# Optimization experiments

Measured on AMD Instinct MI355X. Metric: run time of the kernel, lower is better.

Reference implementation:

```python
import jax, jax.numpy as jnp
import numpy as np

IMAGE_W = 256
IMAGE_H = 256
SIGMA = 0.2
EPS = 1e-07


def _gauss_filter(g, size, psize, pad):
    """g: [B,N] center coords in pixels. Returns [B,N,size,psize]."""
    # grid coords over padded canvas: value i - pad at row i (matches np.indices - pad)
    coords = jnp.arange(size + 2 * pad, dtype=jnp.float32) - pad          # [size+2pad]
    offs = jnp.arange(1, psize + 1, dtype=jnp.float32) - psize / 2 - 0.5  # [psize]
    mu = g[:, :, None] + offs[None, None, :]                              # [B,N,psize]
    F = jnp.exp(-(coords[None, None, :, None] - mu[:, :, None, :]) ** 2 / (2 * SIGMA ** 2))
    F = F / (F.sum(axis=2, keepdims=True) + EPS)
    return F[:, :, pad:size + pad]                                        # [B,N,size,psize]


def setup_inputs() -> dict:
    key = jax.random.key(0)
    k1, k2 = jax.random.split(key)
    brushes = jax.random.uniform(k1, (32, 64, 2), dtype=jnp.float32)
    patches = jax.random.normal(k2, (32, 64, 3, 16, 16), dtype=jnp.float32)
    return {"brushes": brushes, "patches": patches}


def reference(brushes, patches):
    B, N, C, ph, pw = patches.shape
    pad = ph // 2  # pad='half_patch'
    gx = brushes[:, :, 0] * IMAGE_W  # [B,N]
    gy = brushes[:, :, 1] * IMAGE_H
    Fx = _gauss_filter(gx, IMAGE_W, pw, pad)  # [B,N,w,pw]
    Fy = _gauss_filter(gy, IMAGE_H, ph, pad)  # [B,N,h,ph]
    # contract over pw: [B,N,C,w,ph]
    t = jnp.einsum('bnwq,bncpq->bncwp', Fx, patches)
    # contract over ph: [B,N,C,w,h]
    out = jnp.einsum('bncwp,bnhp->bncwh', t, Fy)
    out = out.mean(axis=1)            # [B,C,w,h]
    out = jnp.swapaxes(out, 2, 3)     # [B,C,h,w]
    return out
```

## Files before the change

### kernel.cpp

```cpp
#include <hip/hip_runtime.h>
#include <hip/hip_bf16.h>


#define TILE 16

__global__ __launch_bounds__(256) void brush_tile(
        const float* __restrict__ brushes,
        const float* __restrict__ patches,
        float* __restrict__ out)
{
    const int b   = blockIdx.z;
    const int tx  = blockIdx.x * TILE;
    const int ty  = blockIdx.y * TILE;
    const int tid = threadIdx.x;
    const int qi  = tid & 15;
    const int pi  = tid >> 4;
    const int w   = tx + qi;
    const int h   = ty + pi;

    __shared__ float  gxy[128];
    __shared__ unsigned long long smask;
    __shared__ float  invZ[32];
    __shared__ float4 T4[16 * 21];

    if (tid < 80)
        T4[(tid / 5) * 21 + 16 + (tid % 5)] = make_float4(0, 0, 0, 0);

    if (tid < 64) {
        float2 g = ((const float2*)brushes)[(b << 6) + tid];
        g.x *= 256.0f; g.y *= 256.0f;
        ((float2*)gxy)[tid] = g;
        const bool hit =
            (g.x >= (float)tx - 9.5f) & (g.x <= (float)tx + 24.5f) &
            (g.y >= (float)ty - 9.5f) & (g.y <= (float)ty + 24.5f);
        const unsigned long long m = __ballot(hit);
        if (tid == 0) smask = m;
    }
    __syncthreads();
    unsigned long long mask = smask;

    float acc0 = 0.0f, acc1 = 0.0f, acc2 = 0.0f;
    const float E25 = 1.3887944e-11f;

    while (mask) {
        const int n = __builtin_ctzll(mask);
        mask &= mask - 1;
        const float gx = gxy[2 * n], gy = gxy[2 * n + 1];

        const float* pb = patches + (size_t)((b << 6) + n) * 768;
        const float r0 = pb[tid];
        const float r1 = pb[tid + 256];
        const float r2 = pb[tid + 512];

        if (tid < 32) {
            const int axis = tid >> 4, q = tid & 15;
            const float g  = axis ? gy : gx;
            const float mu = g + (float)q - 7.5f;
            const float fl = floorf(mu);
            float Z = 0.0f;
#pragma unroll
            for (int d = -1; d <= 2; ++d) {
                const float c = fl + (float)d;
                if (c >= -8.0f && c <= 263.0f) {
                    const float u = c - mu;
                    Z += __expf(-12.5f * u * u);
                }
            }
            invZ[tid] = 1.0f / (Z + 1e-7f);
        }
        __syncthreads();

        const float zx = invZ[qi];
        const float v0 = r0 * zx, v1 = r1 * zx, v2 = r2 * zx;

        {
            const float ax  = (float)w - gx + 7.5f;
            const bool  okx = (ax >= -2.5f) & (ax <= 17.5f);
            int qlo = (int)ceilf(ax - 2.0f);
            qlo = qlo < 0 ? 0 : (qlo > 15 ? 15 : qlo);
            float d0 = ax - (float)qlo;
            d0 = fminf(fmaxf(d0, -3.0f), 3.0f);
            float wgt = okx ? __expf(-12.5f * d0 * d0) : 0.0f;
            float u   = __expf(25.0f * d0 - 12.5f);
            const int base = ((pi & 3) << 4) + qlo;
            float4 s = make_float4(0, 0, 0, 0);
#pragma unroll
            for (int j = 0; j < 5; ++j) {
                const float a0 = __shfl(v0, base + j, 64);
                const float a1 = __shfl(v1, base + j, 64);
                const float a2 = __shfl(v2, base + j, 64);
                const float wj = (qlo + j < 16) ? wgt : 0.0f;
                s.x += wj * a0; s.y += wj * a1; s.z += wj * a2;
                wgt *= u; u *= E25;
            }
            const float zy = invZ[16 + pi];
            s.x *= zy; s.y *= zy; s.z *= zy;
            T4[qi * 21 + pi] = s;
        }
        __syncthreads();

        {
            const float ay = (float)h - gy + 7.5f;
            if (ay >= -2.5f && ay <= 17.5f) {
                int plo = (int)ceilf(ay - 2.0f);
                plo = plo < 0 ? 0 : (plo > 15 ? 15 : plo);
                const float d0 = ay - (float)plo;
                float wgt = __expf(-12.5f * d0 * d0);
                float u   = __expf(25.0f * d0 - 12.5f);
                const float4* row = &T4[qi * 21 + plo];
#pragma unroll
                for (int j = 0; j < 5; ++j) {
                    const float4 v = row[j];
                    acc0 += wgt * v.x; acc1 += wgt * v.y; acc2 += wgt * v.z;
                    wgt *= u; u *= E25;
                }
            }
        }
    }

    const float sc = 1.0f / 64.0f;
    float* ob = out + (((size_t)(b * 3)) << 16) + (h << 8) + w;
    ob[0]       = acc0 * sc;
    ob[1 << 16] = acc1 * sc;
    ob[2 << 16] = acc2 * sc;
}

extern "C" void kernel_launch(void* const* d_in, const int* in_sizes, int n_in,
                              void* d_out, int out_size, void* d_ws, size_t ws_size,
                              hipStream_t stream) {
    const float* brushes = (const float*)d_in[0];
    const float* patches = (const float*)d_in[1];
    float* out = (float*)d_out;
    brush_tile<<<dim3(16, 16, 32), dim3(256), 0, stream>>>(brushes, patches, out);
}
```

Measured before the change: 78.54 us.

## Switch from output-tile gather to per-brush scatter with atomic accumulation

Replaces the per-output-tile kernel, which loops over the brushes overlapping each tile, with one block per brush. Each block computes a 22x22 footprint through two separable small contractions in shared memory and accumulates into the output with atomicAdd. A separate zero-fill kernel clears the output first. This removes the serial brush loop and repeated per-tile syncs, at the cost of a second launch, a full output write pass and atomic contention where brushes overlap.

```diff
diff --git a/kernel.cpp b/kernel.cpp
--- a/kernel.cpp
+++ b/kernel.cpp
@@ -1,128 +1,113 @@
 #include <hip/hip_runtime.h>
-#include <hip/hip_bf16.h>
 
 
-#define TILE 16
+__global__ __launch_bounds__(256) void zero_out(float4* __restrict__ out)
+{
+    out[blockIdx.x * 256 + threadIdx.x] = make_float4(0.f, 0.f, 0.f, 0.f);
+}
 
-__global__ __launch_bounds__(256) void brush_tile(
+__global__ __launch_bounds__(256) void brush_scatter(
         const float* __restrict__ brushes,
         const float* __restrict__ patches,
         float* __restrict__ out)
 {
-    const int b   = blockIdx.z;
-    const int tx  = blockIdx.x * TILE;
-    const int ty  = blockIdx.y * TILE;
+    const int n   = blockIdx.x;
+    const int b   = blockIdx.y;
     const int tid = threadIdx.x;
-    const int qi  = tid & 15;
-    const int pi  = tid >> 4;
-    const int w   = tx + qi;
-    const int h   = ty + pi;
 
-    __shared__ float  gxy[128];
-    __shared__ unsigned long long smask;
-    __shared__ float  invZ[32];
-    __shared__ float4 T4[16 * 21];
+    __shared__ float P[3 * 256];
+    __shared__ float wT[2][22][5];
+    __shared__ int   qloT[2][22];
+    __shared__ float T[3 * 352];
 
-    if (tid < 80)
-        T4[(tid / 5) * 21 + 16 + (tid % 5)] = make_float4(0, 0, 0, 0);
+    const int bn = (b << 6) + n;
+    const float gx = brushes[2 * bn]     * 256.0f;
+    const float gy = brushes[2 * bn + 1] * 256.0f;
+    const int x0 = (int)floorf(gx) - 10;
+    const int y0 = (int)floorf(gy) - 10;
 
-    if (tid < 64) {
-        float2 g = ((const float2*)brushes)[(b << 6) + tid];
-        g.x *= 256.0f; g.y *= 256.0f;
-        ((float2*)gxy)[tid] = g;
-        const bool hit =
-            (g.x >= (float)tx - 9.5f) & (g.x <= (float)tx + 24.5f) &
-            (g.y >= (float)ty - 9.5f) & (g.y <= (float)ty + 24.5f);
-        const unsigned long long m = __ballot(hit);
-        if (tid == 0) smask = m;
+    const float* pb = patches + (size_t)bn * 768;
+    P[tid]       = pb[tid];
+    P[tid + 256] = pb[tid + 256];
+    P[tid + 512] = pb[tid + 512];
+
+    if (tid < 220) {
+        const int axis = tid / 110;
+        const int r    = tid - axis * 110;
+        const int i    = r / 5;
+        const int j    = r - i * 5;
+        const float g    = axis ? gy : gx;
+        const float wpos = (float)((axis ? y0 : x0) + i);
+        const float a    = wpos - g + 7.5f;
+        int qlo = (int)ceilf(a - 2.5f);
+        qlo = qlo < 0 ? 0 : (qlo > 11 ? 11 : qlo);
+        const int q = qlo + j;
+        const float mu = g + (float)q - 7.5f;
+        const float fl = floorf(mu);
+        float Z = 0.0f;
+#pragma unroll
+        for (int d = -1; d <= 2; ++d) {
+            const float c = fl + (float)d;
+            if (c >= -8.0f && c <= 263.0f) {
+                const float u = c - mu;
+                Z += __expf(-12.5f * u * u);
+            }
+        }
+        const float dd  = wpos - mu;
+        float wgt = __expf(-12.5f * dd * dd) / (Z + 1e-7f);
+        if (axis == 0) wgt *= 0.015625f;
+        wT[axis][i][j] = wgt;
+        if (j == 0) qloT[axis][i] = qlo;
     }
     __syncthreads();
-    unsigned long long mask = smask;
 
-    float acc0 = 0.0f, acc1 = 0.0f, acc2 = 0.0f;
-    const float E25 = 1.3887944e-11f;
+    for (int it = tid; it < 352; it += 256) {
+        const int p = it / 22;
+        const int i = it - p * 22;
+        const int qlo = qloT[0][i];
+        const float w0 = wT[0][i][0], w1 = wT[0][i][1], w2 = wT[0][i][2],
+                    w3 = wT[0][i][3], w4 = wT[0][i][4];
+        const float* Pp = &P[p * 16 + qlo];
+#pragma unroll
+        for (int c = 0; c < 3; ++c) {
+            const float* Pc = Pp + c * 256;
+            T[c * 352 + p * 22 + i] =
+                w0 * Pc[0] + w1 * Pc[1] + w2 * Pc[2] + w3 * Pc[3] + w4 * Pc[4];
+        }
+    }
+    __syncthreads();
 
-    while (mask) {
-        const int n = __builtin_ctzll(mask);
-        mask &= mask - 1;
-        const float gx = gxy[2 * n], gy = gxy[2 * n + 1];
-
-        const float* pb = patches + (size_t)((b << 6) + n) * 768;
-        const float r0 = pb[tid];
-        const float r1 = pb[tid + 256];
-        const float r2 = pb[tid + 512];
-
-        if (tid < 32) {
-            const int axis = tid >> 4, q = tid & 15;
-            const float g  = axis ? gy : gx;
-            const float mu = g + (float)q - 7.5f;
-            const float fl = floorf(mu);
-            float Z = 0.0f;
-#pragma unroll
-            for (int d = -1; d <= 2; ++d) {
-                const float c = fl + (float)d;
-                if (c >= -8.0f && c <= 263.0f) {
-                    const float u = c - mu;
-                    Z += __expf(-12.5f * u * u);
-                }
+    float* ob = out + ((size_t)(b * 3) << 16);
+    for (int e = tid; e < 484; e += 256) {
+        const int yi = e / 22;
+        const int xi = e - yi * 22;
+        const int h = y0 + yi;
+        const int w = x0 + xi;
+        if (((unsigned)h < 256u) & ((unsigned)w < 256u)) {
+            const int plo = qloT[1][yi];
+            const float w0 = wT[1][yi][0], w1 = wT[1][yi][1], w2 = wT[1][yi][2],
+                        w3 = wT[1][yi][3], w4 = wT[1][yi][4];
+            float v0, v1, v2;
+            {
+                const float* Tc = &T[0 * 352 + plo * 22 + xi];
+                v0 = w0*Tc[0] + w1*Tc[22] + w2*Tc[44] + w3*Tc[66] + w4*Tc[88];
             }
-            invZ[tid] = 1.0f / (Z + 1e-7f);
-        }
-        __syncthreads();
-
-        const float zx = invZ[qi];
-        const float v0 = r0 * zx, v1 = r1 * zx, v2 = r2 * zx;
-
-        {
-            const float ax  = (float)w - gx + 7.5f;
-            const bool  okx = (ax >= -2.5f) & (ax <= 17.5f);
-            int qlo = (int)ceilf(ax - 2.0f);
-            qlo = qlo < 0 ? 0 : (qlo > 15 ? 15 : qlo);
-            float d0 = ax - (float)qlo;
-            d0 = fminf(fmaxf(d0, -3.0f), 3.0f);
-            float wgt = okx ? __expf(-12.5f * d0 * d0) : 0.0f;
-            float u   = __expf(25.0f * d0 - 12.5f);
-            const int base = ((pi & 3) << 4) + qlo;
-            float4 s = make_float4(0, 0, 0, 0);
-#pragma unroll
-            for (int j = 0; j < 5; ++j) {
-                const float a0 = __shfl(v0, base + j, 64);
-                const float a1 = __shfl(v1, base + j, 64);
-                const float a2 = __shfl(v2, base + j, 64);
-                const float wj = (qlo + j < 16) ? wgt : 0.0f;
-                s.x += wj * a0; s.y += wj * a1; s.z += wj * a2;
-                wgt *= u; u *= E25;
+            {
+                const float* Tc = &T[1 * 352 + plo * 22 + xi];
+                v1 = w0*Tc[0] + w1*Tc[22] + w2*Tc[44] + w3*Tc[66] + w4*Tc[88];
             }
-            const float zy = invZ[16 + pi];
-            s.x *= zy; s.y *= zy; s.z *= zy;
-            T4[qi * 21 + pi] = s;
-        }
-        __syncthreads();
-
-        {
-            const float ay = (float)h - gy + 7.5f;
-            if (ay >= -2.5f && ay <= 17.5f) {
-                int plo = (int)ceilf(ay - 2.0f);
-                plo = plo < 0 ? 0 : (plo > 15 ? 15 : plo);
-                const float d0 = ay - (float)plo;
-                float wgt = __expf(-12.5f * d0 * d0);
-                float u   = __expf(25.0f * d0 - 12.5f);
-                const float4* row = &T4[qi * 21 + plo];
-#pragma unroll
-                for (int j = 0; j < 5; ++j) {
-                    const float4 v = row[j];
-                    acc0 += wgt * v.x; acc1 += wgt * v.y; acc2 += wgt * v.z;
-                    wgt *= u; u *= E25;
-                }
+            {
+                const float* Tc = &T[2 * 352 + plo * 22 + xi];
+                v2 = w0*Tc[0] + w1*Tc[22] + w2*Tc[44] + w3*Tc[66] + w4*Tc[88];
+            }
+            if (fabsf(v0) + fabsf(v1) + fabsf(v2) > 1e-12f) {
+                const int off = (h << 8) + w;
+                atomicAdd(ob + off,               v0);
+                atomicAdd(ob + off + (1 << 16),   v1);
+                atomicAdd(ob + off + (2 << 16),   v2);
             }
         }
     }
-
-    const float sc = 1.0f / 64.0f;
-    float* ob = out + (((size_t)(b * 3)) << 16) + (h << 8) + w;
-    ob[0]       = acc0 * sc;
-    ob[1 << 16] = acc1 * sc;
-    ob[2 << 16] = acc2 * sc;
 }
 
 extern "C" void kernel_launch(void* const* d_in, const int* in_sizes, int n_in,
@@ -131,5 +116,6 @@
     const float* brushes = (const float*)d_in[0];
     const float* patches = (const float*)d_in[1];
     float* out = (float*)d_out;
-    brush_tile<<<dim3(16, 16, 32), dim3(256), 0, stream>>>(brushes, patches, out);
+    zero_out<<<dim3(6144), dim3(256), 0, stream>>>((float4*)out);
+    brush_scatter<<<dim3(64, 32), dim3(256), 0, stream>>>(brushes, patches, out);
 }
```

Measured after the change: 81.51 us. 3.8% more time.

## Precompute normalizers for all hit brushes and double-buffer T4 to drop a barrier

Applied to the files above, without the earlier changes.

All normalization factors for the brushes that hit the tile are now computed in parallel before the main loop, using a compacted brush list, instead of by 32 threads inside each iteration. The T4 scratch tile is double-buffered, so each iteration needs one barrier instead of two. Shared memory grows to 8 KB of invZ plus a second T4 buffer, which may reduce occupancy.

```diff
diff --git a/kernel.cpp b/kernel.cpp
--- a/kernel.cpp
+++ b/kernel.cpp
@@ -1,5 +1,4 @@
 #include <hip/hip_runtime.h>
-#include <hip/hip_bf16.h>
 
 
 #define TILE 16
@@ -20,11 +19,14 @@
 
     __shared__ float  gxy[128];
     __shared__ unsigned long long smask;
-    __shared__ float  invZ[32];
-    __shared__ float4 T4[16 * 21];
+    __shared__ unsigned char slist[64];
+    __shared__ float  invZ[64][32];
+    __shared__ float4 T4[2][16 * 21];
 
-    if (tid < 80)
-        T4[(tid / 5) * 21 + 16 + (tid % 5)] = make_float4(0, 0, 0, 0);
+    if (tid < 160) {
+        const int bufi = tid / 80, r = tid - bufi * 80;
+        T4[bufi][(r / 5) * 21 + 16 + (r % 5)] = make_float4(0, 0, 0, 0);
+    }
 
     if (tid < 64) {
         float2 g = ((const float2*)brushes)[(b << 6) + tid];
@@ -34,13 +36,37 @@
             (g.x >= (float)tx - 9.5f) & (g.x <= (float)tx + 24.5f) &
             (g.y >= (float)ty - 9.5f) & (g.y <= (float)ty + 24.5f);
         const unsigned long long m = __ballot(hit);
+        if (hit)
+            slist[__popcll(m & ((1ull << tid) - 1ull))] = (unsigned char)tid;
         if (tid == 0) smask = m;
     }
     __syncthreads();
-    unsigned long long mask = smask;
+    const unsigned long long fullmask = smask;
+    const int cnt = __popcll(fullmask);
+
+    for (int k = tid >> 5; k < cnt; k += 8) {
+        const int n    = slist[k];
+        const int axis = (tid >> 4) & 1, q = tid & 15;
+        const float g  = axis ? gxy[2 * n + 1] : gxy[2 * n];
+        const float mu = g + (float)q - 7.5f;
+        const float fl = floorf(mu);
+        float Z = 0.0f;
+#pragma unroll
+        for (int d = -1; d <= 2; ++d) {
+            const float c = fl + (float)d;
+            if (c >= -8.0f && c <= 263.0f) {
+                const float u = c - mu;
+                Z += __expf(-12.5f * u * u);
+            }
+        }
+        invZ[k][tid & 31] = 1.0f / (Z + 1e-7f);
+    }
+    __syncthreads();
 
     float acc0 = 0.0f, acc1 = 0.0f, acc2 = 0.0f;
     const float E25 = 1.3887944e-11f;
+    unsigned long long mask = fullmask;
+    int k = 0, buf = 0;
 
     while (mask) {
         const int n = __builtin_ctzll(mask);
@@ -52,25 +78,7 @@
         const float r1 = pb[tid + 256];
         const float r2 = pb[tid + 512];
 
-        if (tid < 32) {
-            const int axis = tid >> 4, q = tid & 15;
-            const float g  = axis ? gy : gx;
-            const float mu = g + (float)q - 7.5f;
-            const float fl = floorf(mu);
-            float Z = 0.0f;
-#pragma unroll
-            for (int d = -1; d <= 2; ++d) {
-                const float c = fl + (float)d;
-                if (c >= -8.0f && c <= 263.0f) {
-                    const float u = c - mu;
-                    Z += __expf(-12.5f * u * u);
-                }
-            }
-            invZ[tid] = 1.0f / (Z + 1e-7f);
-        }
-        __syncthreads();
-
-        const float zx = invZ[qi];
+        const float zx = invZ[k][qi];
         const float v0 = r0 * zx, v1 = r1 * zx, v2 = r2 * zx;
 
         {
@@ -93,9 +101,9 @@
                 s.x += wj * a0; s.y += wj * a1; s.z += wj * a2;
                 wgt *= u; u *= E25;
             }
-            const float zy = invZ[16 + pi];
+            const float zy = invZ[k][16 + pi];
             s.x *= zy; s.y *= zy; s.z *= zy;
-            T4[qi * 21 + pi] = s;
+            T4[buf][qi * 21 + pi] = s;
         }
         __syncthreads();
 
@@ -107,7 +115,7 @@
                 const float d0 = ay - (float)plo;
                 float wgt = __expf(-12.5f * d0 * d0);
                 float u   = __expf(25.0f * d0 - 12.5f);
-                const float4* row = &T4[qi * 21 + plo];
+                const float4* row = &T4[buf][qi * 21 + plo];
 #pragma unroll
                 for (int j = 0; j < 5; ++j) {
                     const float4 v = row[j];
@@ -116,6 +124,7 @@
                 }
             }
         }
+        ++k; buf ^= 1;
     }
 
     const float sc = 1.0f / 64.0f;
```

After: 79.68 us. Within noise of the previous version (+1.5%).
